# Kernel optimization log

Measured on AMD Instinct MI355X. Metric: run time of the kernel, lower is better.

The kernel has to match this reference:

```python
import jax, jax.numpy as jnp
import numpy as np

B, N, T, NOUT = 32, 2048, 500, 2
NE = 1638                      # excitatory cells; Ni = N - NE
MUE = 0.5                      # constant external drive
PR = 0.1                       # pr_plastic
DT_TAUSINV = 0.1               # dt / taus_long
WREC_INIT = 1.0 * 10.0 / np.sqrt(N * PR)   # scale_plastic * taum / sqrt(N*pr)


def setup_inputs() -> dict:
    key = jax.random.key(0)
    k1, k2, k3, k4, k5 = jax.random.split(key, 5)
    u0 = jax.random.normal(k1, (B, N), jnp.float32)
    ext = 0.1 * jax.random.normal(k2, (T, B, N), jnp.float32)  # stim+feedback+noise
    mask = (jax.random.uniform(k3, (N, N)) < PR).astype(jnp.float32)
    weight_rec = mask * WREC_INIT * jax.random.uniform(k4, (N, N), jnp.float32)
    weight_sign = jnp.concatenate([jnp.ones(NE, jnp.float32), -jnp.ones(N - NE, jnp.float32)])
    weight_out = 0.1 * jax.random.normal(k5, (N, NOUT), jnp.float32)
    dt_tausinv = jnp.full((1, N), DT_TAUSINV, jnp.float32)
    return dict(u0=u0, ext=ext, weight_rec=weight_rec, mask=mask,
                weight_sign=weight_sign, weight_out=weight_out, dt_tausinv=dt_tausinv)


def reference(u0, ext, weight_rec, mask, weight_sign, weight_out, dt_tausinv):
    # weight_dale(): mask * relu(w_rec) * sign(pre-synaptic cell), applied per column
    w_dale_t = (mask * jax.nn.relu(weight_rec) * weight_sign[None, :]).T  # [N_pre, N_post]

    def step(u, ext_t):
        r = jax.nn.sigmoid(3.0 * u - 2.0)                     # activation(u)
        drive = r @ w_dale_t + MUE + ext_t                    # recurrent + external input
        u_new = u * (1.0 - dt_tausinv) + drive * dt_tausinv   # leaky integration
        out = r @ weight_out                                  # weight_out_mixed readout
        return u_new, (u_new, out)

    _, (usave, outsave) = jax.lax.scan(step, u0, ext)
    return usave, outsave  # [T,B,N], [T,B,Nout]
```

## Files before the change

kernel.cpp:

```cpp
#include <hip/hip_runtime.h>

#define NTOT   2048
#define BATCH  32
#define TSTEPS 500
#define CAP    320
#define RELEMS (BATCH * NTOT)
#define OUT_BASE (TSTEPS * RELEMS)
#define GLOBI  255

static __device__ __forceinline__ float act(float u) {
  return 1.0f / (1.0f + expf(2.0f - 3.0f * u));
}
static __device__ __forceinline__ void st_coh(float* p, float v) {
  __hip_atomic_store(p, v, __ATOMIC_RELAXED, __HIP_MEMORY_SCOPE_AGENT);
}
static __device__ __forceinline__ float ld_coh(const float* p) {
  return __hip_atomic_load(p, __ATOMIC_RELAXED, __HIP_MEMORY_SCOPE_AGENT);
}

__global__ void alif_init(unsigned int* bar) { bar[threadIdx.x] = 0u; }

template <bool FRESH>
__global__ __launch_bounds__(1024, 4) void alif_main(
    const float* __restrict__ u0,
    const float* __restrict__ ext,
    const float* __restrict__ wrec,
    const float* __restrict__ mask,
    const float* __restrict__ sign,
    const float* __restrict__ dtv,
    float* __restrict__ rbuf,
    float* __restrict__ usave,
    unsigned int* __restrict__ bar) {
  const int tid  = threadIdx.x;
  const int lane = tid & 63;
  const int wv   = tid >> 6;
  const int nw   = blockDim.x >> 6;
  const int KR   = NTOT / nw;
  const int cpb  = NTOT / gridDim.x;
  const int lcpb = (cpb == 8) ? 3 : 2;
  const int S    = 32 >> lcpb;
  const int lS   = 5 - lcpb;

  __shared__ uint2 csr[8 * CAP];
  __shared__ float red[32][32];
  __shared__ int   wcnt[16];
  __shared__ int   nnzs[8];
  __shared__ int   maxns;

  for (int clb = 0; clb < cpb; ++clb) {
    const int c = blockIdx.x * cpb + clb;
    const float* __restrict__ mrow = mask + c * NTOT;
    int cnt = 0;
    for (int k0 = wv * KR; k0 < wv * KR + KR; k0 += 64)
      cnt += __popcll(__ballot(mrow[k0 + lane] != 0.0f));
    if (lane == 0) wcnt[wv] = cnt;
    __syncthreads();
    int base = 0, total = 0;
    for (int w2 = 0; w2 < nw; ++w2) {
      if (w2 < wv) base += wcnt[w2];
      total += wcnt[w2];
    }
    for (int k0 = wv * KR; k0 < wv * KR + KR; k0 += 64) {
      const int k = k0 + lane;
      const float mv = mrow[k];
      const bool nz = (mv != 0.0f);
      const unsigned long long bal = __ballot(nz);
      if (nz) {
        const int pos = base + __popcll(bal & ((1ull << lane) - 1ull));
        const float w = mv * fmaxf(wrec[c * NTOT + k], 0.0f) * sign[k];
        if (pos < CAP) csr[clb * CAP + pos] = make_uint2(__float_as_uint(w), (unsigned)(k * BATCH));
      }
      base += __popcll(bal);
    }
    if (tid == 0) nnzs[clb] = (total < CAP) ? total : CAP;
    __syncthreads();
  }
  if (tid == 0) {
    int m = 0;
    for (int i = 0; i < cpb; ++i) m = (nnzs[i] > m) ? nnzs[i] : m;
    const int padm = 8 * S;
    maxns = (m + padm - 1) & ~(padm - 1);
  }
  __syncthreads();
  const int maxn = maxns;
  for (int clb = 0; clb < cpb; ++clb)
    for (int i = nnzs[clb] + tid; i < maxn; i += blockDim.x)
      csr[clb * CAP + i] = make_uint2(0u, 0u);

  const int grp = tid >> 5;
  const int b   = tid & 31;
  const int cl  = grp & (cpb - 1);
  const int s   = grp >> lcpb;
  const int c   = blockIdx.x * cpb + cl;
  const bool own = (s == 0);

  float u = 0.f, dtc = 0.f, omd = 0.f;
  if (own) {
    dtc = dtv[c];
    omd = 1.0f - dtc;
    u = u0[b * NTOT + c];
    st_coh(&rbuf[c * BATCH + b], act(u));
  }
  const unsigned ngrp = gridDim.x >> 5;
  const int g = blockIdx.x & (ngrp - 1);

  for (int t = 0; t < TSTEPS; ++t) {
    __syncthreads();
    if (tid == 0) {
      const unsigned prev =
          __hip_atomic_fetch_add(&bar[16 * g], 1u, __ATOMIC_RELAXED, __HIP_MEMORY_SCOPE_AGENT);
      if (((prev + 1u) & 31u) == 0u)
        __hip_atomic_fetch_add(&bar[GLOBI], 1u, __ATOMIC_RELAXED, __HIP_MEMORY_SCOPE_AGENT);
      const unsigned gt = (unsigned)(t + 1) * ngrp;
      while (__hip_atomic_load(&bar[GLOBI], __ATOMIC_RELAXED, __HIP_MEMORY_SCOPE_AGENT) < gt)
        __builtin_amdgcn_s_sleep(1);
    }
    __syncthreads();

    const float e = own ? ext[(size_t)t * RELEMS + b * NTOT + c] : 0.0f;

    const int Lc = maxn >> lS;
    const uint2* __restrict__ ce = csr + cl * CAP + s * Lc;
    const size_t rph = FRESH ? (size_t)t : (size_t)(t & 1);
    const float* __restrict__ rrow = rbuf + rph * RELEMS + b;
    float a0 = 0.f, a1 = 0.f, a2 = 0.f, a3 = 0.f;
    float a4 = 0.f, a5 = 0.f, a6 = 0.f, a7 = 0.f;
    for (int i = 0; i < Lc; i += 8) {
      const uint2 e0 = ce[i],     e1 = ce[i + 1], e2 = ce[i + 2], e3 = ce[i + 3];
      const uint2 e4 = ce[i + 4], e5 = ce[i + 5], e6 = ce[i + 6], e7 = ce[i + 7];
      if (FRESH) {
        a0 = fmaf(rrow[e0.y], __uint_as_float(e0.x), a0);
        a1 = fmaf(rrow[e1.y], __uint_as_float(e1.x), a1);
        a2 = fmaf(rrow[e2.y], __uint_as_float(e2.x), a2);
        a3 = fmaf(rrow[e3.y], __uint_as_float(e3.x), a3);
        a4 = fmaf(rrow[e4.y], __uint_as_float(e4.x), a4);
        a5 = fmaf(rrow[e5.y], __uint_as_float(e5.x), a5);
        a6 = fmaf(rrow[e6.y], __uint_as_float(e6.x), a6);
        a7 = fmaf(rrow[e7.y], __uint_as_float(e7.x), a7);
      } else {
        a0 = fmaf(ld_coh(rrow + e0.y), __uint_as_float(e0.x), a0);
        a1 = fmaf(ld_coh(rrow + e1.y), __uint_as_float(e1.x), a1);
        a2 = fmaf(ld_coh(rrow + e2.y), __uint_as_float(e2.x), a2);
        a3 = fmaf(ld_coh(rrow + e3.y), __uint_as_float(e3.x), a3);
        a4 = fmaf(ld_coh(rrow + e4.y), __uint_as_float(e4.x), a4);
        a5 = fmaf(ld_coh(rrow + e5.y), __uint_as_float(e5.x), a5);
        a6 = fmaf(ld_coh(rrow + e6.y), __uint_as_float(e6.x), a6);
        a7 = fmaf(ld_coh(rrow + e7.y), __uint_as_float(e7.x), a7);
      }
    }
    red[grp][b] = (((a0 + a1) + (a2 + a3)) + ((a4 + a5) + (a6 + a7)));
    __syncthreads();

    if (own) {
      float rec = 0.f;
      for (int j = 0; j < S; ++j) rec += red[j * cpb + cl][b];
      u = u * omd + ((rec + 0.5f) + e) * dtc;
      const size_t wph = FRESH ? (size_t)(t + 1) : (size_t)((t + 1) & 1);
      st_coh(&rbuf[wph * RELEMS + c * BATCH + b], act(u));
      usave[(size_t)t * RELEMS + b * NTOT + c] = u;
    }
  }
}

__global__ __launch_bounds__(256) void alif_readout(
    const float* __restrict__ u0,
    const float* __restrict__ usave,
    const float* __restrict__ wout,
    float* __restrict__ outs) {
  const int wg = blockIdx.x * 4 + (threadIdx.x >> 6);
  const int lane = threadIdx.x & 63;
  const int t = wg >> 5, b = wg & 31;
  float a0 = 0.f, a1 = 0.f;
  for (int k0 = 0; k0 < NTOT; k0 += 64) {
    const int k = k0 + lane;
    const float uv = (t == 0) ? u0[b * NTOT + k] : usave[(size_t)(t - 1) * RELEMS + b * NTOT + k];
    const float r = act(uv);
    const float2 w2 = *(const float2*)(wout + k * 2);
    a0 = fmaf(r, w2.x, a0);
    a1 = fmaf(r, w2.y, a1);
  }
#pragma unroll
  for (int off = 32; off; off >>= 1) {
    a0 += __shfl_xor(a0, off, 64);
    a1 += __shfl_xor(a1, off, 64);
  }
  if (lane == 0) {
    outs[t * (BATCH * 2) + b * 2 + 0] = a0;
    outs[t * (BATCH * 2) + b * 2 + 1] = a1;
  }
}

extern "C" void kernel_launch(void* const* d_in, const int* in_sizes, int n_in,
                              void* d_out, int out_size, void* d_ws, size_t ws_size,
                              hipStream_t stream) {
  const float* u0   = (const float*)d_in[0];
  const float* ext  = (const float*)d_in[1];
  const float* wrec = (const float*)d_in[2];
  const float* mask = (const float*)d_in[3];
  const float* sign = (const float*)d_in[4];
  const float* wout = (const float*)d_in[5];
  const float* dtv  = (const float*)d_in[6];
  float* out = (float*)d_out;

  char* w = (char*)d_ws;
  unsigned int* bar  = (unsigned int*)w;
  float*        rbuf = (float*)(w + 1024);

  const size_t need = 1024 + (size_t)(TSTEPS + 1) * RELEMS * sizeof(float);
  const bool fresh = (ws_size >= need);

  alif_init<<<dim3(1), dim3(256), 0, stream>>>(bar);

  void* args[] = {(void*)&u0, (void*)&ext, (void*)&wrec, (void*)&mask, (void*)&sign,
                  (void*)&dtv, (void*)&rbuf, (void*)&out, (void*)&bar};

  const void* fn = fresh ? (const void*)alif_main<true> : (const void*)alif_main<false>;

  int G = 256, nb = 0;
  hipError_t oe = fresh
      ? hipOccupancyMaxActiveBlocksPerMultiprocessor(&nb, alif_main<true>, 1024, 0)
      : hipOccupancyMaxActiveBlocksPerMultiprocessor(&nb, alif_main<false>, 1024, 0);
  if (oe == hipSuccess && nb >= 2) G = 512;

  hipError_t err = hipLaunchCooperativeKernel(fn, dim3(G), dim3(1024), args, 0, stream);
  if (err != hipSuccess && G == 512) {
    (void)hipLaunchCooperativeKernel(fn, dim3(256), dim3(1024), args, 0, stream);
  }

  alif_readout<<<dim3(TSTEPS * BATCH / 4), dim3(256), 0, stream>>>(
      u0, out, wout, out + OUT_BASE);
}
```

Before: 2.625 ms.

## Replace global per-step barrier with per-column-group readiness flags

When the full-history buffer is available, the per-timestep global barrier is replaced with per-group counters. Each thread group waits only on the producer groups covering the index range of its own sparse row slice. Per-column padding lengths replace the block-wide max, and padding entries reuse the last index so the range check stays tight. This cuts the time spent waiting on the slowest block each step and lets independent groups run ahead. The cost is more polling of flags, and correctness depends on relaxed atomics giving visibility of the activation stores without an explicit fence.

```diff
diff --git a/kernel.cpp b/kernel.cpp
--- a/kernel.cpp
+++ b/kernel.cpp
@@ -20,7 +20,7 @@
 
 __global__ void alif_init(unsigned int* bar) { bar[threadIdx.x] = 0u; }
 
-template <bool FRESH>
+template <bool PIPE>
 __global__ __launch_bounds__(1024, 4) void alif_main(
     const float* __restrict__ u0,
     const float* __restrict__ ext,
@@ -45,7 +45,7 @@
   __shared__ float red[32][32];
   __shared__ int   wcnt[16];
   __shared__ int   nnzs[8];
-  __shared__ int   maxns;
+  __shared__ int   Lcol[8];
 
   for (int clb = 0; clb < cpb; ++clb) {
     const int c = blockIdx.x * cpb + clb;
@@ -72,27 +72,27 @@
       }
       base += __popcll(bal);
     }
-    if (tid == 0) nnzs[clb] = (total < CAP) ? total : CAP;
-    __syncthreads();
-  }
-  if (tid == 0) {
-    int m = 0;
-    for (int i = 0; i < cpb; ++i) m = (nnzs[i] > m) ? nnzs[i] : m;
-    const int padm = 8 * S;
-    maxns = (m + padm - 1) & ~(padm - 1);
-  }
-  __syncthreads();
-  const int maxn = maxns;
-  for (int clb = 0; clb < cpb; ++clb)
-    for (int i = nnzs[clb] + tid; i < maxn; i += blockDim.x)
-      csr[clb * CAP + i] = make_uint2(0u, 0u);
+    if (tid == 0) {
+      const int nn = (total < CAP) ? total : CAP;
+      nnzs[clb] = nn;
+      const int padm = 8 * S;
+      Lcol[clb] = (nn + padm - 1) & ~(padm - 1);
+    }
+    __syncthreads();
+  }
+  for (int clb = 0; clb < cpb; ++clb) {
+    const int nn = nnzs[clb];
+    const unsigned ylast = (nn > 0) ? csr[clb * CAP + nn - 1].y : 0u;
+    for (int i = nn + tid; i < Lcol[clb]; i += blockDim.x)
+      csr[clb * CAP + i] = make_uint2(0u, ylast);
+  }
 
   const int grp = tid >> 5;
   const int b   = tid & 31;
   const int cl  = grp & (cpb - 1);
   const int s   = grp >> lcpb;
   const int c   = blockIdx.x * cpb + cl;
-  const bool own = (s == 0);
+  const bool own = (grp < cpb);
 
   float u = 0.f, dtc = 0.f, omd = 0.f;
   if (own) {
@@ -101,51 +101,73 @@
     u = u0[b * NTOT + c];
     st_coh(&rbuf[c * BATCH + b], act(u));
   }
-  const unsigned ngrp = gridDim.x >> 5;
-  const int g = blockIdx.x & (ngrp - 1);
+  const unsigned ngrpc = gridDim.x >> 5;
+  const int Gc   = blockIdx.x >> 5;
+  const int gfb  = blockIdx.x & (ngrpc - 1);
+  const int shf  = 5 + (31 - __clz((unsigned)(NTOT / ngrpc)));
 
   for (int t = 0; t < TSTEPS; ++t) {
     __syncthreads();
-    if (tid == 0) {
-      const unsigned prev =
-          __hip_atomic_fetch_add(&bar[16 * g], 1u, __ATOMIC_RELAXED, __HIP_MEMORY_SCOPE_AGENT);
-      if (((prev + 1u) & 31u) == 0u)
-        __hip_atomic_fetch_add(&bar[GLOBI], 1u, __ATOMIC_RELAXED, __HIP_MEMORY_SCOPE_AGENT);
-      const unsigned gt = (unsigned)(t + 1) * ngrp;
-      while (__hip_atomic_load(&bar[GLOBI], __ATOMIC_RELAXED, __HIP_MEMORY_SCOPE_AGENT) < gt)
-        __builtin_amdgcn_s_sleep(1);
-    }
-    __syncthreads();
+    if (PIPE) {
+      if (tid == 0) {
+        const unsigned prev =
+            __hip_atomic_fetch_add(&bar[128 + 8 * Gc], 1u, __ATOMIC_RELAXED, __HIP_MEMORY_SCOPE_AGENT);
+        if (((prev + 1u) & 31u) == 0u)
+          __hip_atomic_store(&bar[8 * Gc], (prev + 1u) >> 5,
+                             __ATOMIC_RELAXED, __HIP_MEMORY_SCOPE_AGENT);
+      }
+    } else {
+      if (tid == 0) {
+        const unsigned prev =
+            __hip_atomic_fetch_add(&bar[16 * gfb], 1u, __ATOMIC_RELAXED, __HIP_MEMORY_SCOPE_AGENT);
+        if (((prev + 1u) & 31u) == 0u)
+          __hip_atomic_fetch_add(&bar[GLOBI], 1u, __ATOMIC_RELAXED, __HIP_MEMORY_SCOPE_AGENT);
+        const unsigned gt = (unsigned)(t + 1) * ngrpc;
+        while (__hip_atomic_load(&bar[GLOBI], __ATOMIC_RELAXED, __HIP_MEMORY_SCOPE_AGENT) < gt)
+          __builtin_amdgcn_s_sleep(1);
+      }
+      __syncthreads();
+    }
 
     const float e = own ? ext[(size_t)t * RELEMS + b * NTOT + c] : 0.0f;
 
-    const int Lc = maxn >> lS;
+    const int Lc = Lcol[cl] >> lS;
     const uint2* __restrict__ ce = csr + cl * CAP + s * Lc;
-    const size_t rph = FRESH ? (size_t)t : (size_t)(t & 1);
-    const float* __restrict__ rrow = rbuf + rph * RELEMS + b;
     float a0 = 0.f, a1 = 0.f, a2 = 0.f, a3 = 0.f;
     float a4 = 0.f, a5 = 0.f, a6 = 0.f, a7 = 0.f;
-    for (int i = 0; i < Lc; i += 8) {
-      const uint2 e0 = ce[i],     e1 = ce[i + 1], e2 = ce[i + 2], e3 = ce[i + 3];
-      const uint2 e4 = ce[i + 4], e5 = ce[i + 5], e6 = ce[i + 6], e7 = ce[i + 7];
-      if (FRESH) {
-        a0 = fmaf(rrow[e0.y], __uint_as_float(e0.x), a0);
-        a1 = fmaf(rrow[e1.y], __uint_as_float(e1.x), a1);
-        a2 = fmaf(rrow[e2.y], __uint_as_float(e2.x), a2);
-        a3 = fmaf(rrow[e3.y], __uint_as_float(e3.x), a3);
-        a4 = fmaf(rrow[e4.y], __uint_as_float(e4.x), a4);
-        a5 = fmaf(rrow[e5.y], __uint_as_float(e5.x), a5);
-        a6 = fmaf(rrow[e6.y], __uint_as_float(e6.x), a6);
-        a7 = fmaf(rrow[e7.y], __uint_as_float(e7.x), a7);
-      } else {
-        a0 = fmaf(ld_coh(rrow + e0.y), __uint_as_float(e0.x), a0);
-        a1 = fmaf(ld_coh(rrow + e1.y), __uint_as_float(e1.x), a1);
-        a2 = fmaf(ld_coh(rrow + e2.y), __uint_as_float(e2.x), a2);
-        a3 = fmaf(ld_coh(rrow + e3.y), __uint_as_float(e3.x), a3);
-        a4 = fmaf(ld_coh(rrow + e4.y), __uint_as_float(e4.x), a4);
-        a5 = fmaf(ld_coh(rrow + e5.y), __uint_as_float(e5.x), a5);
-        a6 = fmaf(ld_coh(rrow + e6.y), __uint_as_float(e6.x), a6);
-        a7 = fmaf(ld_coh(rrow + e7.y), __uint_as_float(e7.x), a7);
+    if (Lc > 0) {
+      if (PIPE) {
+        const unsigned jlo = ce[0].y >> shf;
+        const unsigned jhi = ce[Lc - 1].y >> shf;
+        const unsigned tgt = (unsigned)(t + 1);
+        for (unsigned j = jlo; j <= jhi; ++j)
+          while (__hip_atomic_load(&bar[8 * j], __ATOMIC_RELAXED, __HIP_MEMORY_SCOPE_AGENT) < tgt)
+            __builtin_amdgcn_s_sleep(1);
+      }
+      const size_t rph = PIPE ? (size_t)t : (size_t)(t & 1);
+      const float* __restrict__ rrow = rbuf + rph * RELEMS + b;
+      for (int i = 0; i < Lc; i += 8) {
+        const uint2 e0 = ce[i],     e1 = ce[i + 1], e2 = ce[i + 2], e3 = ce[i + 3];
+        const uint2 e4 = ce[i + 4], e5 = ce[i + 5], e6 = ce[i + 6], e7 = ce[i + 7];
+        if (PIPE) {
+          a0 = fmaf(rrow[e0.y], __uint_as_float(e0.x), a0);
+          a1 = fmaf(rrow[e1.y], __uint_as_float(e1.x), a1);
+          a2 = fmaf(rrow[e2.y], __uint_as_float(e2.x), a2);
+          a3 = fmaf(rrow[e3.y], __uint_as_float(e3.x), a3);
+          a4 = fmaf(rrow[e4.y], __uint_as_float(e4.x), a4);
+          a5 = fmaf(rrow[e5.y], __uint_as_float(e5.x), a5);
+          a6 = fmaf(rrow[e6.y], __uint_as_float(e6.x), a6);
+          a7 = fmaf(rrow[e7.y], __uint_as_float(e7.x), a7);
+        } else {
+          a0 = fmaf(ld_coh(rrow + e0.y), __uint_as_float(e0.x), a0);
+          a1 = fmaf(ld_coh(rrow + e1.y), __uint_as_float(e1.x), a1);
+          a2 = fmaf(ld_coh(rrow + e2.y), __uint_as_float(e2.x), a2);
+          a3 = fmaf(ld_coh(rrow + e3.y), __uint_as_float(e3.x), a3);
+          a4 = fmaf(ld_coh(rrow + e4.y), __uint_as_float(e4.x), a4);
+          a5 = fmaf(ld_coh(rrow + e5.y), __uint_as_float(e5.x), a5);
+          a6 = fmaf(ld_coh(rrow + e6.y), __uint_as_float(e6.x), a6);
+          a7 = fmaf(ld_coh(rrow + e7.y), __uint_as_float(e7.x), a7);
+        }
       }
     }
     red[grp][b] = (((a0 + a1) + (a2 + a3)) + ((a4 + a5) + (a6 + a7)));
@@ -155,7 +177,7 @@
       float rec = 0.f;
       for (int j = 0; j < S; ++j) rec += red[j * cpb + cl][b];
       u = u * omd + ((rec + 0.5f) + e) * dtc;
-      const size_t wph = FRESH ? (size_t)(t + 1) : (size_t)((t + 1) & 1);
+      const size_t wph = PIPE ? (size_t)(t + 1) : (size_t)((t + 1) & 1);
       st_coh(&rbuf[wph * RELEMS + c * BATCH + b], act(u));
       usave[(size_t)t * RELEMS + b * NTOT + c] = u;
     }
```

Result: slower. 3.349 ms (+27.6%).
